# Kernel tuning notes

Measured on AMD Instinct MI355X. Metric: run time of the kernel, lower is better.

The kernel has to match this reference:

```python
import jax, jax.numpy as jnp
import numpy as np

B, S, H = 32, 1024, 512  # batch, src_len, hidden_dim


def setup_inputs() -> dict:
    key = jax.random.key(0)
    k1, k2, k3, k4, k5 = jax.random.split(key, 5)
    hidden = jax.random.normal(k1, (B, H), dtype=jnp.float32)
    encoder_outputs = jax.random.normal(k2, (B, S, 2 * H), dtype=jnp.float32)
    # nn.Linear(3H, H): weight stored here as [3H, H] (input-major) with bias [H]
    W = jax.random.normal(k3, (3 * H, H), dtype=jnp.float32) / np.sqrt(3 * H)
    b = jax.random.normal(k4, (H,), dtype=jnp.float32) * 0.01
    v = jax.random.normal(k5, (H,), dtype=jnp.float32) / np.sqrt(H)
    return {"hidden": hidden, "encoder_outputs": encoder_outputs, "W": W, "b": b, "v": v}


def reference(hidden, encoder_outputs, W, b, v):
    # concat((repeat(hidden), encoder_outputs)) @ W  ==  hidden @ W[:H] (broadcast) + enc @ W[H:]
    Wh, We = W[:H], W[H:]                         # [H,H], [2H,H]
    h_proj = hidden @ Wh                           # [B,H]
    e_proj = jnp.einsum('bse,eh->bsh', encoder_outputs, We)  # [B,S,H]
    energy = jnp.tanh(h_proj[:, None, :] + e_proj + b)       # [B,S,H]
    # bmm(v[B,1,H], energy^T[B,H,S]) -> scores [B,S]
    scores = jnp.einsum('bsh,h->bs', energy, v)
    return jax.nn.softmax(scores, axis=1)
```

## Files before the change

kernel.cpp:

```cpp
#include <hip/hip_runtime.h>
#include <math.h>

#define B_ 32
#define S_ 1024
#define H_ 512
#define K_ 1024
#define M_ (B_ * S_)

typedef __attribute__((ext_vector_type(8))) short bf16x8;
typedef __attribute__((ext_vector_type(16))) float f32x16;

__device__ __forceinline__ void split_bf16(float f, unsigned short& hi, unsigned short& lo) {
    unsigned u = __float_as_uint(f);
    unsigned r = u + 0x8000u;
    hi = (unsigned short)(r >> 16);
    float fh = __uint_as_float(r & 0xffff0000u);
    float res = f - fh;
    lo = (unsigned short)((__float_as_uint(res) + 0x8000u) >> 16);
}

__device__ __forceinline__ void split8_store(const float4& x, const float4& y,
                                             unsigned short* hiP, unsigned short* loP) {
    float f[8] = {x.x, x.y, x.z, x.w, y.x, y.y, y.z, y.w};
    unsigned hr[8], lr[8];
    #pragma unroll
    for (int i = 0; i < 8; ++i) {
        unsigned u = __float_as_uint(f[i]);
        unsigned r = u + 0x8000u;
        hr[i] = r;
        float fh = __uint_as_float(r & 0xffff0000u);
        lr[i] = __float_as_uint(f[i] - fh) + 0x8000u;
    }
    uint4 Hv, Lv;
    Hv.x = __builtin_amdgcn_perm(hr[1], hr[0], 0x07060302u);
    Hv.y = __builtin_amdgcn_perm(hr[3], hr[2], 0x07060302u);
    Hv.z = __builtin_amdgcn_perm(hr[5], hr[4], 0x07060302u);
    Hv.w = __builtin_amdgcn_perm(hr[7], hr[6], 0x07060302u);
    Lv.x = __builtin_amdgcn_perm(lr[1], lr[0], 0x07060302u);
    Lv.y = __builtin_amdgcn_perm(lr[3], lr[2], 0x07060302u);
    Lv.z = __builtin_amdgcn_perm(lr[5], lr[4], 0x07060302u);
    Lv.w = __builtin_amdgcn_perm(lr[7], lr[6], 0x07060302u);
    *reinterpret_cast<uint4*>(hiP) = Hv;
    *reinterpret_cast<uint4*>(loP) = Lv;
}

__device__ __forceinline__ float fast_tanh(float x) {
    float xc = fminf(fmaxf(x, -15.f), 15.f);
    float t = __expf(2.0f * xc);
    return (t - 1.0f) * __builtin_amdgcn_rcpf(t + 1.0f);
}

__device__ __forceinline__ void async_copy16(const void* g, void* l) {
    __builtin_amdgcn_global_load_lds(
        (const __attribute__((address_space(1))) void*)g,
        (__attribute__((address_space(3))) void*)l, 16, 0, 0);
}

__global__ __launch_bounds__(256) void prep_kernel(
    const float* __restrict__ hidden, const float* __restrict__ W,
    const float* __restrict__ bias, float* __restrict__ hb,
    unsigned short* __restrict__ Wh, unsigned short* __restrict__ Wl)
{
    __shared__ float red[4][64];
    __shared__ float t[32][33];
    const int bx = blockIdx.x;
    if (bx < 256) {
        const int tid = threadIdx.x;
        const int h0  = (bx & 7) * 64;
        const int b   = bx >> 3;
        const int h   = h0 + (tid & 63);
        const int ks  = tid >> 6;
        const float* hrow = hidden + b * H_;
        float acc = 0.f;
        #pragma unroll 8
        for (int k = ks * 128; k < ks * 128 + 128; ++k)
            acc = fmaf(hrow[k], W[(size_t)k * H_ + h], acc);
        red[ks][tid & 63] = acc;
        __syncthreads();
        if (tid < 64)
            hb[b * H_ + h0 + tid] = red[0][tid] + red[1][tid] + red[2][tid]
                                  + red[3][tid] + bias[h0 + tid];
    } else {
        const float* We = W + (size_t)H_ * H_;
        const int cx = bx - 256;
        const int k0 = (cx & 31) * 32, n0 = (cx >> 5) * 32;
        const int tx = threadIdx.x & 31, ty = threadIdx.x >> 5;
        #pragma unroll
        for (int j = 0; j < 4; ++j) {
            const int k = ty + 8 * j;
            t[k][tx] = We[(size_t)(k0 + k) * H_ + n0 + tx];
        }
        __syncthreads();
        #pragma unroll
        for (int j = 0; j < 4; ++j) {
            const int n    = ty + 8 * j;
            const int ncol = n0 + n;
            const int k    = k0 + tx;
            unsigned short hi, lo;
            split_bf16(t[tx][n], hi, lo);
            const int c     = ncol >> 5;
            const int tt    = k >> 4;
            const int lane_ = ((k >> 3) & 1) * 32 + (ncol & 31);
            const size_t s  = ((size_t)(c * 64 + tt) * 64 + lane_) * 8 + (k & 7);
            Wh[s] = hi;
            Wl[s] = lo;
        }
    }
}

__global__ __launch_bounds__(512, 2) void gemm_fused(
    const float* __restrict__ EO,
    const unsigned short* __restrict__ Bth,
    const unsigned short* __restrict__ Btl,
    const float* __restrict__ hb, const float* __restrict__ v,
    float* __restrict__ partial)
{
    __shared__ unsigned short ldsA[2][2][8192];
    __shared__ unsigned short ldsB[3][2][8192];

    const int tid  = threadIdx.x;
    const int bid  = blockIdx.x;
    const int jb   = bid >> 3;
    const int mt   = (bid & 7) * 16 + (jb >> 1);
    const int nt   = jb & 1;
    const int row0 = mt * 256;
    const int col0 = nt * 256;
    const int batch = row0 >> 10;

    const int lane   = tid & 63;
    const int wave   = tid >> 6;
    const int wm     = wave >> 2, wn = wave & 3;
    const int lane32 = lane & 31, kh = lane >> 5;

    size_t gA[2];
    int offAw[2];
    #pragma unroll
    for (int s = 0; s < 2; ++s) {
        const int seg = tid + 512 * s;
        const int m = seg >> 2, sg = seg & 3;
        gA[s]    = (size_t)(row0 + m) * K_ + sg * 8;
        offAw[s] = ((m >> 5) * 2 + (sg >> 1)) * 512
                 + ((sg & 1) * 32 + ((m & 31) ^ sg)) * 8;
    }
    const unsigned short* gBh = Bth + ((size_t)(nt * 8 + wave) * 32768 + lane * 8);
    const unsigned short* gBl = Btl + ((size_t)(nt * 8 + wave) * 32768 + lane * 8);
    const int offBw = wave * 1024;

    f32x16 acc[4][2];
    #pragma unroll
    for (int fi = 0; fi < 4; ++fi)
        #pragma unroll
        for (int fj = 0; fj < 2; ++fj)
            #pragma unroll
            for (int e = 0; e < 16; ++e)
                acc[fi][fj][e] = 0.f;

    float4 a0[2], a1[2];
    #pragma unroll
    for (int s = 0; s < 2; ++s) {
        a0[s] = *reinterpret_cast<const float4*>(EO + gA[s]);
        a1[s] = *reinterpret_cast<const float4*>(EO + gA[s] + 4);
    }
    #pragma unroll
    for (int ks = 0; ks < 2; ++ks) {
        async_copy16(gBh + (0 + ks) * 512, &ldsB[0][0][offBw + ks * 512]);
        async_copy16(gBl + (0 + ks) * 512, &ldsB[0][1][offBw + ks * 512]);
    }
    #pragma unroll
    for (int ks = 0; ks < 2; ++ks) {
        async_copy16(gBh + (2 + ks) * 512, &ldsB[1][0][offBw + ks * 512]);
        async_copy16(gBl + (2 + ks) * 512, &ldsB[1][1][offBw + ks * 512]);
    }
    #pragma unroll
    for (int s = 0; s < 2; ++s)
        split8_store(a0[s], a1[s], &ldsA[0][0][offAw[s]], &ldsA[0][1][offAw[s]]);
    asm volatile("s_waitcnt vmcnt(4) lgkmcnt(0)" ::: "memory");
    __builtin_amdgcn_s_barrier();

#define PHASE_MFMA(fb)                                                         \
    _Pragma("unroll") for (int ks = 0; ks < 2; ++ks)                           \
      _Pragma("unroll") for (int p = 0; p < 3; ++p)                            \
        _Pragma("unroll") for (int f2 = 0; f2 < 2; ++f2)                       \
          _Pragma("unroll") for (int fj = 0; fj < 2; ++fj) {                   \
            acc[(fb) + f2][fj] = __builtin_amdgcn_mfma_f32_32x32x16_bf16(      \
                (p == 2) ? a_l[f2][ks] : a_h[f2][ks],                          \
                (p == 1) ? b_l[fj][ks] : b_h[fj][ks],                          \
                acc[(fb) + f2][fj], 0, 0, 0);                                  \
          }

    int bc = 0;
    for (int j = 0; j < 32; ++j) {
        const int cur = j & 1, nxt = cur ^ 1;
        const int bn  = (bc >= 1) ? bc - 1 : 2;

        bf16x8 b_h[2][2], b_l[2][2];
        #pragma unroll
        for (int fj = 0; fj < 2; ++fj)
            #pragma unroll
            for (int ks = 0; ks < 2; ++ks) {
                const int baseB = ((wn * 2 + fj) * 2 + ks) * 512 + lane * 8;
                b_h[fj][ks] = *reinterpret_cast<const bf16x8*>(&ldsB[bc][0][baseB]);
                b_l[fj][ks] = *reinterpret_cast<const bf16x8*>(&ldsB[bc][1][baseB]);
            }
        {
            bf16x8 a_h[2][2], a_l[2][2];
            #pragma unroll
            for (int f2 = 0; f2 < 2; ++f2)
                #pragma unroll
                for (int ks = 0; ks < 2; ++ks) {
                    const int baseA = ((wm * 4 + f2) * 2 + ks) * 512
                                    + (kh * 32 + (lane32 ^ (2 * ks + kh))) * 8;
                    a_h[f2][ks] = *reinterpret_cast<const bf16x8*>(&ldsA[cur][0][baseA]);
                    a_l[f2][ks] = *reinterpret_cast<const bf16x8*>(&ldsA[cur][1][baseA]);
                }
            if (j < 31) {
                const int k0n = 32 * (j + 1);
                #pragma unroll
                for (int s = 0; s < 2; ++s) {
                    a0[s] = *reinterpret_cast<const float4*>(EO + gA[s] + k0n);
                    a1[s] = *reinterpret_cast<const float4*>(EO + gA[s] + k0n + 4);
                }
            }
            __builtin_amdgcn_s_barrier();
            asm volatile("s_waitcnt lgkmcnt(0)" ::: "memory");
            __builtin_amdgcn_sched_barrier(0);
            __builtin_amdgcn_s_setprio(1);
            PHASE_MFMA(0)
            __builtin_amdgcn_s_setprio(0);
            __builtin_amdgcn_s_barrier();
        }

        {
            bf16x8 a_h[2][2], a_l[2][2];
            #pragma unroll
            for (int f2 = 0; f2 < 2; ++f2)
                #pragma unroll
                for (int ks = 0; ks < 2; ++ks) {
                    const int baseA = ((wm * 4 + 2 + f2) * 2 + ks) * 512
                                    + (kh * 32 + (lane32 ^ (2 * ks + kh))) * 8;
                    a_h[f2][ks] = *reinterpret_cast<const bf16x8*>(&ldsA[cur][0][baseA]);
                    a_l[f2][ks] = *reinterpret_cast<const bf16x8*>(&ldsA[cur][1][baseA]);
                }
            if (j < 30) {
                const int tnxt = 2 * (j + 2);
                #pragma unroll
                for (int ks = 0; ks < 2; ++ks) {
                    async_copy16(gBh + (tnxt + ks) * 512, &ldsB[bn][0][offBw + ks * 512]);
                    async_copy16(gBl + (tnxt + ks) * 512, &ldsB[bn][1][offBw + ks * 512]);
                }
            }
            if (j < 31) {
                #pragma unroll
                for (int s = 0; s < 2; ++s)
                    split8_store(a0[s], a1[s],
                                 &ldsA[nxt][0][offAw[s]], &ldsA[nxt][1][offAw[s]]);
            }
            __builtin_amdgcn_s_barrier();
            asm volatile("s_waitcnt lgkmcnt(0)" ::: "memory");
            __builtin_amdgcn_sched_barrier(0);
            __builtin_amdgcn_s_setprio(1);
            PHASE_MFMA(2)
            __builtin_amdgcn_s_setprio(0);
            asm volatile("s_waitcnt vmcnt(4)" ::: "memory");
            __builtin_amdgcn_s_barrier();
        }
        bc = (bc == 2) ? 0 : bc + 1;
    }
#undef PHASE_MFMA

    const float* hb_row = hb + batch * H_;
    float hbv[2], vv[2];
    #pragma unroll
    for (int fj = 0; fj < 2; ++fj) {
        const int c = col0 + (wn * 2 + fj) * 32 + lane32;
        hbv[fj] = hb_row[c];
        vv[fj]  = v[c];
    }
    float* red = reinterpret_cast<float*>(&ldsA[0][0][0]);
    #pragma unroll
    for (int fi = 0; fi < 4; ++fi)
        #pragma unroll
        for (int r = 0; r < 16; ++r) {
            float rs = 0.f;
            #pragma unroll
            for (int fj = 0; fj < 2; ++fj)
                rs = fmaf(fast_tanh(acc[fi][fj][r] + hbv[fj]), vv[fj], rs);
            rs += __shfl_xor(rs, 1, 64);
            rs += __shfl_xor(rs, 2, 64);
            rs += __shfl_xor(rs, 4, 64);
            rs += __shfl_xor(rs, 8, 64);
            rs += __shfl_xor(rs, 16, 64);
            if (lane32 == 0) {
                const int row = wm * 128 + fi * 32 + (r & 3) + 8 * (r >> 2) + 4 * kh;
                red[row * 4 + wn] = rs;
            }
        }
    __syncthreads();
    if (tid < 256)
        partial[(size_t)nt * M_ + row0 + tid] =
            red[tid * 4] + red[tid * 4 + 1] + red[tid * 4 + 2] + red[tid * 4 + 3];
}

__global__ __launch_bounds__(256) void softmax_kernel(
    const float* __restrict__ partial, float* __restrict__ out)
{
    const int b = blockIdx.x;
    const int tid = threadIdx.x;
    float val[4];
    float lmax = -3.0e38f;
    #pragma unroll
    for (int q = 0; q < 4; ++q) {
        const int idx = b * S_ + tid + 256 * q;
        float sum = partial[idx] + partial[M_ + idx];
        val[q] = sum;
        lmax = fmaxf(lmax, sum);
    }
    #pragma unroll
    for (int off = 32; off > 0; off >>= 1)
        lmax = fmaxf(lmax, __shfl_down(lmax, off, 64));
    __shared__ float wmax[4];
    if ((tid & 63) == 0) wmax[tid >> 6] = lmax;
    __syncthreads();
    const float gmax = fmaxf(fmaxf(wmax[0], wmax[1]), fmaxf(wmax[2], wmax[3]));
    float lsum = 0.0f;
    #pragma unroll
    for (int q = 0; q < 4; ++q) {
        val[q] = expf(val[q] - gmax);
        lsum += val[q];
    }
    #pragma unroll
    for (int off = 32; off > 0; off >>= 1)
        lsum += __shfl_down(lsum, off, 64);
    __shared__ float wsum[4];
    if ((tid & 63) == 0) wsum[tid >> 6] = lsum;
    __syncthreads();
    const float inv = 1.0f / (wsum[0] + wsum[1] + wsum[2] + wsum[3]);
    #pragma unroll
    for (int q = 0; q < 4; ++q)
        out[b * S_ + tid + 256 * q] = val[q] * inv;
}

extern "C" void kernel_launch(void* const* d_in, const int* in_sizes, int n_in,
                              void* d_out, int out_size, void* d_ws, size_t ws_size,
                              hipStream_t stream) {
    const float* hidden = (const float*)d_in[0];
    const float* EO     = (const float*)d_in[1];
    const float* W      = (const float*)d_in[2];
    const float* bias   = (const float*)d_in[3];
    const float* v      = (const float*)d_in[4];
    float* out          = (float*)d_out;

    float* hb      = (float*)d_ws;
    float* partial = hb + B_ * H_;
    unsigned short* Wth = (unsigned short*)(partial + 4 * M_);
    unsigned short* Wtl = Wth + (size_t)H_ * K_;

    prep_kernel<<<768, 256, 0, stream>>>(hidden, W, bias, hb, Wth, Wtl);
    gemm_fused<<<dim3(256), 512, 0, stream>>>(EO, Wth, Wtl, hb, v, partial);
    softmax_kernel<<<B_, 256, 0, stream>>>(partial, out);
}
```

Baseline: 292.5 us.

## Pre-split encoder outputs to bf16 hi/lo in prep and DMA both GEMM operands

Moves the fp32-to-bf16 hi/lo split of the encoder outputs out of the GEMM main loop into extra prep_kernel blocks, which write pre-tiled A operands to the workspace. The new gemm_dma kernel then loads A through global_load_lds async copies exactly like B, so its main loop no longer does register loads and split/store work. The cost is an extra full pass over the 128MB input plus writing and rereading a 128MB bf16 pair. A fallback gemm_fb kernel with a restructured single-phase loop runs when the workspace is too small.

```diff
diff --git a/kernel.cpp b/kernel.cpp
--- a/kernel.cpp
+++ b/kernel.cpp
@@ -57,9 +57,11 @@
 }
 
 __global__ __launch_bounds__(256) void prep_kernel(
-    const float* __restrict__ hidden, const float* __restrict__ W,
-    const float* __restrict__ bias, float* __restrict__ hb,
-    unsigned short* __restrict__ Wh, unsigned short* __restrict__ Wl)
+    const float* __restrict__ hidden, const float* __restrict__ EO,
+    const float* __restrict__ W, const float* __restrict__ bias,
+    float* __restrict__ hb,
+    unsigned short* __restrict__ Wh, unsigned short* __restrict__ Wl,
+    unsigned short* __restrict__ Ah, unsigned short* __restrict__ Al)
 {
     __shared__ float red[4][64];
     __shared__ float t[32][33];
@@ -80,7 +82,7 @@
         if (tid < 64)
             hb[b * H_ + h0 + tid] = red[0][tid] + red[1][tid] + red[2][tid]
                                   + red[3][tid] + bias[h0 + tid];
-    } else {
+    } else if (bx < 768) {
         const float* We = W + (size_t)H_ * H_;
         const int cx = bx - 256;
         const int k0 = (cx & 31) * 32, n0 = (cx >> 5) * 32;
@@ -105,77 +107,23 @@
             Wh[s] = hi;
             Wl[s] = lo;
         }
-    }
-}
-
-__global__ __launch_bounds__(512, 2) void gemm_fused(
-    const float* __restrict__ EO,
-    const unsigned short* __restrict__ Bth,
-    const unsigned short* __restrict__ Btl,
-    const float* __restrict__ hb, const float* __restrict__ v,
-    float* __restrict__ partial)
-{
-    __shared__ unsigned short ldsA[2][2][8192];
-    __shared__ unsigned short ldsB[3][2][8192];
-
-    const int tid  = threadIdx.x;
-    const int bid  = blockIdx.x;
-    const int jb   = bid >> 3;
-    const int mt   = (bid & 7) * 16 + (jb >> 1);
-    const int nt   = jb & 1;
-    const int row0 = mt * 256;
-    const int col0 = nt * 256;
-    const int batch = row0 >> 10;
-
-    const int lane   = tid & 63;
-    const int wave   = tid >> 6;
-    const int wm     = wave >> 2, wn = wave & 3;
-    const int lane32 = lane & 31, kh = lane >> 5;
-
-    size_t gA[2];
-    int offAw[2];
-    #pragma unroll
-    for (int s = 0; s < 2; ++s) {
-        const int seg = tid + 512 * s;
-        const int m = seg >> 2, sg = seg & 3;
-        gA[s]    = (size_t)(row0 + m) * K_ + sg * 8;
-        offAw[s] = ((m >> 5) * 2 + (sg >> 1)) * 512
-                 + ((sg & 1) * 32 + ((m & 31) ^ sg)) * 8;
-    }
-    const unsigned short* gBh = Bth + ((size_t)(nt * 8 + wave) * 32768 + lane * 8);
-    const unsigned short* gBl = Btl + ((size_t)(nt * 8 + wave) * 32768 + lane * 8);
-    const int offBw = wave * 1024;
-
-    f32x16 acc[4][2];
-    #pragma unroll
-    for (int fi = 0; fi < 4; ++fi)
-        #pragma unroll
-        for (int fj = 0; fj < 2; ++fj)
-            #pragma unroll
-            for (int e = 0; e < 16; ++e)
-                acc[fi][fj][e] = 0.f;
-
-    float4 a0[2], a1[2];
-    #pragma unroll
-    for (int s = 0; s < 2; ++s) {
-        a0[s] = *reinterpret_cast<const float4*>(EO + gA[s]);
-        a1[s] = *reinterpret_cast<const float4*>(EO + gA[s] + 4);
-    }
-    #pragma unroll
-    for (int ks = 0; ks < 2; ++ks) {
-        async_copy16(gBh + (0 + ks) * 512, &ldsB[0][0][offBw + ks * 512]);
-        async_copy16(gBl + (0 + ks) * 512, &ldsB[0][1][offBw + ks * 512]);
-    }
-    #pragma unroll
-    for (int ks = 0; ks < 2; ++ks) {
-        async_copy16(gBh + (2 + ks) * 512, &ldsB[1][0][offBw + ks * 512]);
-        async_copy16(gBl + (2 + ks) * 512, &ldsB[1][1][offBw + ks * 512]);
-    }
-    #pragma unroll
-    for (int s = 0; s < 2; ++s)
-        split8_store(a0[s], a1[s], &ldsA[0][0][offAw[s]], &ldsA[0][1][offAw[s]]);
-    asm volatile("s_waitcnt vmcnt(4) lgkmcnt(0)" ::: "memory");
-    __builtin_amdgcn_s_barrier();
+    } else {
+        const int gw   = (bx - 768) * 4 + (threadIdx.x >> 6);
+        const int lane = threadIdx.x & 63;
+        const int lr   = lane >> 2, lc = lane & 3;
+        #pragma unroll 1
+        for (int tt = gw; tt < 65536; tt += 8192) {
+            const int rt = tt >> 5, kt = tt & 31;
+            const int m  = rt * 16 + lr;
+            const int k0 = kt * 32 + lc * 8;
+            const float4 x = *reinterpret_cast<const float4*>(EO + (size_t)m * K_ + k0);
+            const float4 y = *reinterpret_cast<const float4*>(EO + (size_t)m * K_ + k0 + 4);
+            const size_t off = (((size_t)(m >> 5) * 64 + (k0 >> 4)) * 64
+                               + ((k0 >> 3) & 1) * 32 + (m & 31)) * 8;
+            split8_store(x, y, Ah + off, Al + off);
+        }
+    }
+}
 
 #define PHASE_MFMA(fb)                                                         \
     _Pragma("unroll") for (int ks = 0; ks < 2; ++ks)                           \
@@ -188,12 +136,70 @@
                 acc[(fb) + f2][fj], 0, 0, 0);                                  \
           }
 
+__global__ __launch_bounds__(512, 2) void gemm_dma(
+    const unsigned short* __restrict__ Ath,
+    const unsigned short* __restrict__ Atl,
+    const unsigned short* __restrict__ Bth,
+    const unsigned short* __restrict__ Btl,
+    const float* __restrict__ hb, const float* __restrict__ v,
+    float* __restrict__ partial)
+{
+    __shared__ unsigned short ldsA[2][2][8192];
+    __shared__ unsigned short ldsB[3][2][8192];
+
+    const int tid  = threadIdx.x;
+    const int bid  = blockIdx.x;
+    const int jb   = bid >> 3;
+    const int mt   = (bid & 7) * 16 + (jb >> 1);
+    const int nt   = jb & 1;
+    const int row0 = mt * 256;
+    const int col0 = nt * 256;
+    const int batch = row0 >> 10;
+
+    const int lane   = tid & 63;
+    const int wave   = tid >> 6;
+    const int wm     = wave >> 2, wn = wave & 3;
+    const int lane32 = lane & 31, kh = lane >> 5;
+
+    const unsigned short* gAh = Ath + ((size_t)(mt * 8 + wave) * 32768) + lane * 8;
+    const unsigned short* gAl = Atl + ((size_t)(mt * 8 + wave) * 32768) + lane * 8;
+    const unsigned short* gBh = Bth + ((size_t)(nt * 8 + wave) * 32768) + lane * 8;
+    const unsigned short* gBl = Btl + ((size_t)(nt * 8 + wave) * 32768) + lane * 8;
+    const int offW = wave * 1024;
+
+    f32x16 acc[4][2];
+    #pragma unroll
+    for (int fi = 0; fi < 4; ++fi)
+        #pragma unroll
+        for (int fj = 0; fj < 2; ++fj)
+            #pragma unroll
+            for (int e = 0; e < 16; ++e)
+                acc[fi][fj][e] = 0.f;
+
+    #pragma unroll
+    for (int ks = 0; ks < 2; ++ks) {
+        async_copy16(gAh + ks * 512, &ldsA[0][0][offW + ks * 512]);
+        async_copy16(gAl + ks * 512, &ldsA[0][1][offW + ks * 512]);
+    }
+    #pragma unroll
+    for (int ks = 0; ks < 2; ++ks) {
+        async_copy16(gBh + ks * 512, &ldsB[0][0][offW + ks * 512]);
+        async_copy16(gBl + ks * 512, &ldsB[0][1][offW + ks * 512]);
+    }
+    #pragma unroll
+    for (int ks = 0; ks < 2; ++ks) {
+        async_copy16(gBh + (2 + ks) * 512, &ldsB[1][0][offW + ks * 512]);
+        async_copy16(gBl + (2 + ks) * 512, &ldsB[1][1][offW + ks * 512]);
+    }
+    asm volatile("s_waitcnt vmcnt(4)" ::: "memory");
+    __builtin_amdgcn_s_barrier();
+
     int bc = 0;
     for (int j = 0; j < 32; ++j) {
         const int cur = j & 1, nxt = cur ^ 1;
         const int bn  = (bc >= 1) ? bc - 1 : 2;
 
-        bf16x8 b_h[2][2], b_l[2][2];
+        bf16x8 b_h[2][2], b_l[2][2], a_h[2][2], a_l[2][2];
         #pragma unroll
         for (int fj = 0; fj < 2; ++fj)
             #pragma unroll
@@ -202,71 +208,57 @@
                 b_h[fj][ks] = *reinterpret_cast<const bf16x8*>(&ldsB[bc][0][baseB]);
                 b_l[fj][ks] = *reinterpret_cast<const bf16x8*>(&ldsB[bc][1][baseB]);
             }
-        {
-            bf16x8 a_h[2][2], a_l[2][2];
-            #pragma unroll
-            for (int f2 = 0; f2 < 2; ++f2)
-                #pragma unroll
-                for (int ks = 0; ks < 2; ++ks) {
-                    const int baseA = ((wm * 4 + f2) * 2 + ks) * 512
-                                    + (kh * 32 + (lane32 ^ (2 * ks + kh))) * 8;
-                    a_h[f2][ks] = *reinterpret_cast<const bf16x8*>(&ldsA[cur][0][baseA]);
-                    a_l[f2][ks] = *reinterpret_cast<const bf16x8*>(&ldsA[cur][1][baseA]);
-                }
-            if (j < 31) {
-                const int k0n = 32 * (j + 1);
-                #pragma unroll
-                for (int s = 0; s < 2; ++s) {
-                    a0[s] = *reinterpret_cast<const float4*>(EO + gA[s] + k0n);
-                    a1[s] = *reinterpret_cast<const float4*>(EO + gA[s] + k0n + 4);
-                }
-            }
-            __builtin_amdgcn_s_barrier();
-            asm volatile("s_waitcnt lgkmcnt(0)" ::: "memory");
-            __builtin_amdgcn_sched_barrier(0);
-            __builtin_amdgcn_s_setprio(1);
-            PHASE_MFMA(0)
-            __builtin_amdgcn_s_setprio(0);
-            __builtin_amdgcn_s_barrier();
-        }
-
-        {
-            bf16x8 a_h[2][2], a_l[2][2];
-            #pragma unroll
-            for (int f2 = 0; f2 < 2; ++f2)
-                #pragma unroll
-                for (int ks = 0; ks < 2; ++ks) {
-                    const int baseA = ((wm * 4 + 2 + f2) * 2 + ks) * 512
-                                    + (kh * 32 + (lane32 ^ (2 * ks + kh))) * 8;
-                    a_h[f2][ks] = *reinterpret_cast<const bf16x8*>(&ldsA[cur][0][baseA]);
-                    a_l[f2][ks] = *reinterpret_cast<const bf16x8*>(&ldsA[cur][1][baseA]);
-                }
-            if (j < 30) {
-                const int tnxt = 2 * (j + 2);
-                #pragma unroll
-                for (int ks = 0; ks < 2; ++ks) {
-                    async_copy16(gBh + (tnxt + ks) * 512, &ldsB[bn][0][offBw + ks * 512]);
-                    async_copy16(gBl + (tnxt + ks) * 512, &ldsB[bn][1][offBw + ks * 512]);
-                }
-            }
-            if (j < 31) {
-                #pragma unroll
-                for (int s = 0; s < 2; ++s)
-                    split8_store(a0[s], a1[s],
-                                 &ldsA[nxt][0][offAw[s]], &ldsA[nxt][1][offAw[s]]);
-            }
-            __builtin_amdgcn_s_barrier();
-            asm volatile("s_waitcnt lgkmcnt(0)" ::: "memory");
-            __builtin_amdgcn_sched_barrier(0);
-            __builtin_amdgcn_s_setprio(1);
-            PHASE_MFMA(2)
-            __builtin_amdgcn_s_setprio(0);
-            asm volatile("s_waitcnt vmcnt(4)" ::: "memory");
-            __builtin_amdgcn_s_barrier();
-        }
+        #pragma unroll
+        for (int f2 = 0; f2 < 2; ++f2)
+            #pragma unroll
+            for (int ks = 0; ks < 2; ++ks) {
+                const int baseA = ((wm * 4 + f2) * 2 + ks) * 512 + lane * 8;
+                a_h[f2][ks] = *reinterpret_cast<const bf16x8*>(&ldsA[cur][0][baseA]);
+                a_l[f2][ks] = *reinterpret_cast<const bf16x8*>(&ldsA[cur][1][baseA]);
+            }
+        if (j < 31) {
+            const int t16 = 2 * (j + 1);
+            #pragma unroll
+            for (int ks = 0; ks < 2; ++ks) {
+                async_copy16(gAh + (t16 + ks) * 512, &ldsA[nxt][0][offW + ks * 512]);
+                async_copy16(gAl + (t16 + ks) * 512, &ldsA[nxt][1][offW + ks * 512]);
+            }
+        }
+        __builtin_amdgcn_s_barrier();
+        asm volatile("s_waitcnt lgkmcnt(0)" ::: "memory");
+        __builtin_amdgcn_sched_barrier(0);
+        __builtin_amdgcn_s_setprio(1);
+        PHASE_MFMA(0)
+        __builtin_amdgcn_s_setprio(0);
+        __builtin_amdgcn_s_barrier();
+
+        #pragma unroll
+        for (int f2 = 0; f2 < 2; ++f2)
+            #pragma unroll
+            for (int ks = 0; ks < 2; ++ks) {
+                const int baseA = ((wm * 4 + 2 + f2) * 2 + ks) * 512 + lane * 8;
+                a_h[f2][ks] = *reinterpret_cast<const bf16x8*>(&ldsA[cur][0][baseA]);
+                a_l[f2][ks] = *reinterpret_cast<const bf16x8*>(&ldsA[cur][1][baseA]);
+            }
+        if (j < 30) {
+            const int t16 = 2 * (j + 2);
+            #pragma unroll
+            for (int ks = 0; ks < 2; ++ks) {
+                async_copy16(gBh + (t16 + ks) * 512, &ldsB[bn][0][offW + ks * 512]);
+                async_copy16(gBl + (t16 + ks) * 512, &ldsB[bn][1][offW + ks * 512]);
+            }
+        }
+        __builtin_amdgcn_s_barrier();
+        asm volatile("s_waitcnt lgkmcnt(0)" ::: "memory");
+        __builtin_amdgcn_sched_barrier(0);
+        __builtin_amdgcn_s_setprio(1);
+        PHASE_MFMA(2)
+        __builtin_amdgcn_s_setprio(0);
+        if (j < 30)       { asm volatile("s_waitcnt vmcnt(4)" ::: "memory"); }
+        else if (j == 30) { asm volatile("s_waitcnt vmcnt(0)" ::: "memory"); }
+        __builtin_amdgcn_s_barrier();
         bc = (bc == 2) ? 0 : bc + 1;
     }
-#undef PHASE_MFMA
 
     const float* hb_row = hb + batch * H_;
     float hbv[2], vv[2];
@@ -301,6 +293,178 @@
             red[tid * 4] + red[tid * 4 + 1] + red[tid * 4 + 2] + red[tid * 4 + 3];
 }
 
+__global__ __launch_bounds__(512, 2) void gemm_fb(
+    const float* __restrict__ EO,
+    const unsigned short* __restrict__ Bth, const unsigned short* __restrict__ Btl,
+    const float* __restrict__ hb, const float* __restrict__ v,
+    float* __restrict__ partial)
+{
+    __shared__ unsigned short ldsA[2][2][8192];
+    __shared__ unsigned short ldsB[3][2][8192];
+
+    const int tid  = threadIdx.x;
+    const int bid  = blockIdx.x;
+    const int jb   = bid >> 3;
+    const int mt   = (bid & 7) * 16 + (jb >> 1);
+    const int nt   = jb & 1;
+    const int row0 = mt * 256;
+    const int col0 = nt * 256;
+    const int batch = row0 >> 10;
+
+    const int lane   = tid & 63;
+    const int wave   = tid >> 6;
+    const int wm     = wave >> 2, wn = wave & 3;
+    const int lane32 = lane & 31, kh = lane >> 5;
+
+    size_t gA[2];
+    int offAw[2];
+    #pragma unroll
+    for (int s = 0; s < 2; ++s) {
+        const int seg = tid + 512 * s;
+        const int m = seg >> 2, sg = seg & 3;
+        gA[s]    = (size_t)(row0 + m) * K_ + sg * 8;
+        offAw[s] = ((m >> 5) * 2 + (sg >> 1)) * 512
+                 + ((sg & 1) * 32 + ((m & 31) ^ sg)) * 8;
+    }
+    const unsigned short* gBh = Bth + ((size_t)(nt * 8 + wave) * 32768 + lane * 8);
+    const unsigned short* gBl = Btl + ((size_t)(nt * 8 + wave) * 32768 + lane * 8);
+    const int offBw = wave * 1024;
+
+    f32x16 acc[4][2];
+    #pragma unroll
+    for (int fi = 0; fi < 4; ++fi)
+        #pragma unroll
+        for (int fj = 0; fj < 2; ++fj)
+            #pragma unroll
+            for (int e = 0; e < 16; ++e)
+                acc[fi][fj][e] = 0.f;
+
+    float4 a0[2], a1[2];
+    #pragma unroll
+    for (int s = 0; s < 2; ++s) {
+        a0[s] = *reinterpret_cast<const float4*>(EO + gA[s]);
+        a1[s] = *reinterpret_cast<const float4*>(EO + gA[s] + 4);
+    }
+    #pragma unroll
+    for (int s = 0; s < 2; ++s)
+        split8_store(a0[s], a1[s], &ldsA[0][0][offAw[s]], &ldsA[0][1][offAw[s]]);
+    #pragma unroll
+    for (int ks = 0; ks < 2; ++ks) {
+        async_copy16(gBh + ks * 512, &ldsB[0][0][offBw + ks * 512]);
+        async_copy16(gBl + ks * 512, &ldsB[0][1][offBw + ks * 512]);
+    }
+    #pragma unroll
+    for (int ks = 0; ks < 2; ++ks) {
+        async_copy16(gBh + (2 + ks) * 512, &ldsB[1][0][offBw + ks * 512]);
+        async_copy16(gBl + (2 + ks) * 512, &ldsB[1][1][offBw + ks * 512]);
+    }
+    asm volatile("s_waitcnt vmcnt(4) lgkmcnt(0)\n\ts_barrier" ::: "memory");
+
+    int bc = 0;
+    for (int j = 0; j < 32; ++j) {
+        const int cur = j & 1, nxt = cur ^ 1;
+        const int bn  = (bc >= 1) ? bc - 1 : 2;
+
+        if (j < 31) {
+            const int k0n = 32 * (j + 1);
+            #pragma unroll
+            for (int s = 0; s < 2; ++s) {
+                a0[s] = *reinterpret_cast<const float4*>(EO + gA[s] + k0n);
+                a1[s] = *reinterpret_cast<const float4*>(EO + gA[s] + k0n + 4);
+            }
+        }
+        if (j < 30) {
+            const int tnxt = 2 * (j + 2);
+            #pragma unroll
+            for (int ks = 0; ks < 2; ++ks) {
+                async_copy16(gBh + (tnxt + ks) * 512, &ldsB[bn][0][offBw + ks * 512]);
+                async_copy16(gBl + (tnxt + ks) * 512, &ldsB[bn][1][offBw + ks * 512]);
+            }
+        }
+
+        __builtin_amdgcn_s_setprio(1);
+        bf16x8 b_h[2][2], b_l[2][2];
+        #pragma unroll
+        for (int fj = 0; fj < 2; ++fj)
+            #pragma unroll
+            for (int ks = 0; ks < 2; ++ks) {
+                const int baseB = ((wn * 2 + fj) * 2 + ks) * 512 + lane * 8;
+                b_h[fj][ks] = *reinterpret_cast<const bf16x8*>(&ldsB[bc][0][baseB]);
+                b_l[fj][ks] = *reinterpret_cast<const bf16x8*>(&ldsB[bc][1][baseB]);
+            }
+        #pragma unroll
+        for (int fi = 0; fi < 4; ++fi) {
+            bf16x8 a_h[2], a_l[2];
+            #pragma unroll
+            for (int ks = 0; ks < 2; ++ks) {
+                const int baseA = ((wm * 4 + fi) * 2 + ks) * 512
+                                + (kh * 32 + (lane32 ^ (2 * ks + kh))) * 8;
+                a_h[ks] = *reinterpret_cast<const bf16x8*>(&ldsA[cur][0][baseA]);
+                a_l[ks] = *reinterpret_cast<const bf16x8*>(&ldsA[cur][1][baseA]);
+            }
+            #pragma unroll
+            for (int fj = 0; fj < 2; ++fj)
+                #pragma unroll
+                for (int ks = 0; ks < 2; ++ks) {
+                    acc[fi][fj] = __builtin_amdgcn_mfma_f32_32x32x16_bf16(
+                        a_h[ks], b_h[fj][ks], acc[fi][fj], 0, 0, 0);
+                    acc[fi][fj] = __builtin_amdgcn_mfma_f32_32x32x16_bf16(
+                        a_h[ks], b_l[fj][ks], acc[fi][fj], 0, 0, 0);
+                    acc[fi][fj] = __builtin_amdgcn_mfma_f32_32x32x16_bf16(
+                        a_l[ks], b_h[fj][ks], acc[fi][fj], 0, 0, 0);
+                }
+        }
+        __builtin_amdgcn_s_setprio(0);
+
+        if (j < 30) {
+            #pragma unroll
+            for (int s = 0; s < 2; ++s)
+                split8_store(a0[s], a1[s],
+                             &ldsA[nxt][0][offAw[s]], &ldsA[nxt][1][offAw[s]]);
+            asm volatile("s_waitcnt vmcnt(4) lgkmcnt(0)\n\ts_barrier" ::: "memory");
+        } else if (j == 30) {
+            #pragma unroll
+            for (int s = 0; s < 2; ++s)
+                split8_store(a0[s], a1[s],
+                             &ldsA[nxt][0][offAw[s]], &ldsA[nxt][1][offAw[s]]);
+            asm volatile("s_waitcnt vmcnt(0) lgkmcnt(0)\n\ts_barrier" ::: "memory");
+        }
+        bc = (bc == 2) ? 0 : bc + 1;
+    }
+
+    const float* hb_row = hb + batch * H_;
+    float hbv[2], vv[2];
+    #pragma unroll
+    for (int fj = 0; fj < 2; ++fj) {
+        const int c = col0 + (wn * 2 + fj) * 32 + lane32;
+        hbv[fj] = hb_row[c];
+        vv[fj]  = v[c];
+    }
+    float* red = reinterpret_cast<float*>(&ldsA[0][0][0]);
+    #pragma unroll
+    for (int fi = 0; fi < 4; ++fi)
+        #pragma unroll
+        for (int r = 0; r < 16; ++r) {
+            float rs = 0.f;
+            #pragma unroll
+            for (int fj = 0; fj < 2; ++fj)
+                rs = fmaf(fast_tanh(acc[fi][fj][r] + hbv[fj]), vv[fj], rs);
+            rs += __shfl_xor(rs, 1, 64);
+            rs += __shfl_xor(rs, 2, 64);
+            rs += __shfl_xor(rs, 4, 64);
+            rs += __shfl_xor(rs, 8, 64);
+            rs += __shfl_xor(rs, 16, 64);
+            if (lane32 == 0) {
+                const int row = wm * 128 + fi * 32 + (r & 3) + 8 * (r >> 2) + 4 * kh;
+                red[row * 4 + wn] = rs;
+            }
+        }
+    __syncthreads();
+    if (tid < 256)
+        partial[(size_t)nt * M_ + row0 + tid] =
+            red[tid * 4] + red[tid * 4 + 1] + red[tid * 4 + 2] + red[tid * 4 + 3];
+}
+
 __global__ __launch_bounds__(256) void softmax_kernel(
     const float* __restrict__ partial, float* __restrict__ out)
 {
@@ -354,8 +518,21 @@
     float* partial = hb + B_ * H_;
     unsigned short* Wth = (unsigned short*)(partial + 4 * M_);
     unsigned short* Wtl = Wth + (size_t)H_ * K_;
-
-    prep_kernel<<<768, 256, 0, stream>>>(hidden, W, bias, hb, Wth, Wtl);
-    gemm_fused<<<dim3(256), 512, 0, stream>>>(EO, Wth, Wtl, hb, v, partial);
+    unsigned short* Ath = Wtl + (size_t)H_ * K_;
+    unsigned short* Atl = Ath + (size_t)M_ * K_;
+
+    const size_t need = (size_t)(B_ * H_ + 4 * M_) * sizeof(float)
+                      + (size_t)H_ * K_ * 2 * sizeof(unsigned short)
+                      + (size_t)M_ * K_ * 2 * sizeof(unsigned short);
+
+    if (ws_size >= need) {
+        prep_kernel<<<2816, 256, 0, stream>>>(hidden, EO, W, bias, hb,
+                                              Wth, Wtl, Ath, Atl);
+        gemm_dma<<<dim3(256), 512, 0, stream>>>(Ath, Atl, Wth, Wtl, hb, v, partial);
+    } else {
+        prep_kernel<<<768, 256, 0, stream>>>(hidden, EO, W, bias, hb,
+                                             Wth, Wtl, Ath, Atl);
+        gemm_fb<<<dim3(256), 512, 0, stream>>>(EO, Wth, Wtl, hb, v, partial);
+    }
     softmax_kernel<<<B_, 256, 0, stream>>>(partial, out);
 }
```

Measured after the change: 319.0 us. 1.09x slower.
